# Kernel optimization log

Hardware: AMD Instinct MI355X
Metric: run time of the kernel (lower is better)

The kernel has to match this reference:

```python
import jax, jax.numpy as jnp
import numpy as np

B, S, D, H = 2, 2048, 1024, 16
DEPTH = D // H


def setup_inputs() -> dict:
    key = jax.random.key(0)
    ks = jax.random.split(key, 10)
    scale = 1.0 / np.sqrt(D)
    x = jax.random.normal(ks[0], (B, S, D), dtype=jnp.float32)
    # Astromer-style float mask: values in [0,1], shape (B, S, 1)
    mask = jax.random.uniform(ks[1], (B, S, 1), dtype=jnp.float32)
    Wq = jax.random.normal(ks[2], (D, D), dtype=jnp.float32) * scale
    bq = jnp.zeros((D,), dtype=jnp.float32)
    Wk = jax.random.normal(ks[3], (D, D), dtype=jnp.float32) * scale
    bk = jnp.zeros((D,), dtype=jnp.float32)
    Wv = jax.random.normal(ks[4], (D, D), dtype=jnp.float32) * scale
    bv = jnp.zeros((D,), dtype=jnp.float32)
    Wo = jax.random.normal(ks[5], (D, D), dtype=jnp.float32) * scale
    bo = jnp.zeros((D,), dtype=jnp.float32)
    return {"x": x, "mask": mask, "Wq": Wq, "bq": bq, "Wk": Wk, "bk": bk,
            "Wv": Wv, "bv": bv, "Wo": Wo, "bo": bo}


def _split_heads(t):
    # (B, S, D) -> (B, H, S, depth)
    b, s, _ = t.shape
    return t.reshape(b, s, H, DEPTH).transpose(0, 2, 1, 3)


def reference(x, mask, Wq, bq, Wk, bk, Wv, bv, Wo, bo):
    b, s, d = x.shape
    q = _split_heads(x @ Wq + bq)  # (B,H,S,depth)
    k = _split_heads(x @ Wk + bk)
    v = _split_heads(x @ Wv + bv)
    logits = jnp.einsum('bhqd,bhkd->bhqk', q, k) / jnp.sqrt(
        jnp.asarray(DEPTH, dtype=x.dtype))
    # symmetric mask: tile (B,S,1) -> (B,S,S), add transpose, clamp at 1
    m = jnp.broadcast_to(mask, (b, s, s))  # tile along last dim
    m = m + m.transpose(0, 2, 1)
    m = jnp.minimum(1.0, m)
    logits = logits + m[:, None, :, :]  # broadcast over heads
    attn = jax.nn.softmax(logits, axis=-1)
    z = jnp.einsum('bhqk,bhkd->bhqd', attn, v)
    z = z.transpose(0, 2, 1, 3).reshape(b, s, d)
    out = z @ Wo + bo
    return out, attn
```

## Files before the change

### kernel.cpp

```cpp
#include <hip/hip_runtime.h>

#define B_ 2
#define S_ 2048
#define D_ 1024
#define H_ 16
#define DEPTH_ 64

#define SWZ(g, d) ((((g) ^ ((d) & 15)) << 2))

__global__ __launch_bounds__(256, 2) void gemm128(
    const float* __restrict__ A, const float* __restrict__ Bw,
    const float* __restrict__ bias, float* __restrict__ C)
{
    __shared__ float As[16][132];
    __shared__ float Bs[16][132];
    int t = threadIdx.x;
    int row0 = blockIdx.y * 128, col0 = blockIdx.x * 128;

    int ar = t >> 2, ak = (t & 3) << 2;
    int bk = t >> 5, bc = (t & 31) << 2;
    int tm = (t >> 4) << 3, tn = (t & 15) << 3;

    float acc[8][8] = {};

    for (int k0 = 0; k0 < 1024; k0 += 16) {
        float4 a0 = *(const float4*)(A + (long)(row0 + ar) * 1024 + k0 + ak);
        float4 a1 = *(const float4*)(A + (long)(row0 + ar + 64) * 1024 + k0 + ak);
        float4 b0 = *(const float4*)(Bw + (long)(k0 + bk) * 1024 + col0 + bc);
        float4 b1 = *(const float4*)(Bw + (long)(k0 + bk + 8) * 1024 + col0 + bc);
        As[ak + 0][ar] = a0.x; As[ak + 1][ar] = a0.y;
        As[ak + 2][ar] = a0.z; As[ak + 3][ar] = a0.w;
        As[ak + 0][ar + 64] = a1.x; As[ak + 1][ar + 64] = a1.y;
        As[ak + 2][ar + 64] = a1.z; As[ak + 3][ar + 64] = a1.w;
        *(float4*)&Bs[bk][bc] = b0;
        *(float4*)&Bs[bk + 8][bc] = b1;
        __syncthreads();
#pragma unroll
        for (int kk = 0; kk < 16; ++kk) {
            float4 x0 = *(const float4*)&As[kk][tm];
            float4 x1 = *(const float4*)&As[kk][tm + 4];
            float4 y0 = *(const float4*)&Bs[kk][tn];
            float4 y1 = *(const float4*)&Bs[kk][tn + 4];
            float xa[8] = {x0.x, x0.y, x0.z, x0.w, x1.x, x1.y, x1.z, x1.w};
            float yb[8] = {y0.x, y0.y, y0.z, y0.w, y1.x, y1.y, y1.z, y1.w};
#pragma unroll
            for (int i = 0; i < 8; ++i)
#pragma unroll
                for (int j = 0; j < 8; ++j) acc[i][j] += xa[i] * yb[j];
        }
        __syncthreads();
    }

    float4 bv0 = *(const float4*)(bias + col0 + tn);
    float4 bv1 = *(const float4*)(bias + col0 + tn + 4);
#pragma unroll
    for (int i = 0; i < 8; ++i) {
        float4 o0, o1;
        o0.x = acc[i][0] + bv0.x; o0.y = acc[i][1] + bv0.y;
        o0.z = acc[i][2] + bv0.z; o0.w = acc[i][3] + bv0.w;
        o1.x = acc[i][4] + bv1.x; o1.y = acc[i][5] + bv1.y;
        o1.z = acc[i][6] + bv1.z; o1.w = acc[i][7] + bv1.w;
        float* cp = C + (long)(row0 + tm + i) * 1024 + col0;
        *(float4*)(cp + tn) = o0;
        *(float4*)(cp + tn + 4) = o1;
    }
}

__global__ __launch_bounds__(256, 2) void scores(
    const float* __restrict__ q, const float* __restrict__ k,
    const float* __restrict__ mask, float* __restrict__ attn)
{
    __shared__ float Qs[64 * 64];
    __shared__ float Ks[64 * 64];
    int t = threadIdx.x;
    int bh = blockIdx.z, b = bh >> 4, h = bh & 15;
    int q0 = blockIdx.y * 64, k0 = blockIdx.x * 64;

    int rr = t >> 4, c4 = (t & 15) << 2;
    const float* qb = q + (long)(b * S_ + q0) * D_ + h * DEPTH_;
    const float* kb = k + (long)(b * S_ + k0) * D_ + h * DEPTH_;
#pragma unroll
    for (int i = 0; i < 4; ++i) {
        int r = rr + 16 * i;
        float4 qv = *(const float4*)(qb + (long)r * D_ + c4);
        float4 kv = *(const float4*)(kb + (long)r * D_ + c4);
        int g = r >> 2, e = r & 3;
        Qs[(c4 + 0) * 64 + SWZ(g, c4 + 0) + e] = qv.x;
        Qs[(c4 + 1) * 64 + SWZ(g, c4 + 1) + e] = qv.y;
        Qs[(c4 + 2) * 64 + SWZ(g, c4 + 2) + e] = qv.z;
        Qs[(c4 + 3) * 64 + SWZ(g, c4 + 3) + e] = qv.w;
        Ks[(c4 + 0) * 64 + SWZ(g, c4 + 0) + e] = kv.x;
        Ks[(c4 + 1) * 64 + SWZ(g, c4 + 1) + e] = kv.y;
        Ks[(c4 + 2) * 64 + SWZ(g, c4 + 2) + e] = kv.z;
        Ks[(c4 + 3) * 64 + SWZ(g, c4 + 3) + e] = kv.w;
    }
    __syncthreads();

    int tm = (t >> 4) << 2, tn = (t & 15) << 2;
    int gm = tm >> 2, gn = tn >> 2;
    float acc[4][4] = {};
#pragma unroll
    for (int kk = 0; kk < 64; ++kk) {
        float4 qa = *(const float4*)&Qs[kk * 64 + SWZ(gm, kk)];
        float4 kv = *(const float4*)&Ks[kk * 64 + SWZ(gn, kk)];
        float xa[4] = {qa.x, qa.y, qa.z, qa.w};
        float yb[4] = {kv.x, kv.y, kv.z, kv.w};
#pragma unroll
        for (int i = 0; i < 4; ++i)
#pragma unroll
            for (int j = 0; j < 4; ++j) acc[i][j] += xa[i] * yb[j];
    }

    float mq[4];
#pragma unroll
    for (int i = 0; i < 4; ++i) mq[i] = mask[b * S_ + q0 + tm + i];
    float4 mk4 = *(const float4*)(mask + b * S_ + k0 + tn);
    float mk[4] = {mk4.x, mk4.y, mk4.z, mk4.w};
    float* op = attn + (long)bh * S_ * S_;
#pragma unroll
    for (int i = 0; i < 4; ++i) {
        float4 o;
        o.x = acc[i][0] * 0.125f + fminf(1.0f, mq[i] + mk[0]);
        o.y = acc[i][1] * 0.125f + fminf(1.0f, mq[i] + mk[1]);
        o.z = acc[i][2] * 0.125f + fminf(1.0f, mq[i] + mk[2]);
        o.w = acc[i][3] * 0.125f + fminf(1.0f, mq[i] + mk[3]);
        *(float4*)(op + (long)(q0 + tm + i) * S_ + k0 + tn) = o;
    }
}

__global__ __launch_bounds__(256, 2) void attn_av(
    float* __restrict__ attn, const float* __restrict__ v, float* __restrict__ z)
{
    __shared__ float Ps[64 * 64];
    __shared__ float Vs[64 * 64];
    __shared__ float m_s[64], linv_s[64];

    int t = threadIdx.x;
    int bh = blockIdx.y, b = bh >> 4, h = bh & 15;
    int q0 = blockIdx.x * 64;
    float* arow = attn + (long)bh * S_ * S_;

    int wv = t >> 6, lane = t & 63;
    for (int rr = 0; rr < 16; ++rr) {
        int r = wv * 16 + rr;
        const float* rowp = arow + (long)(q0 + r) * S_;
        float4 x[8];
#pragma unroll
        for (int j = 0; j < 8; ++j)
            x[j] = *(const float4*)(rowp + 4 * lane + 256 * j);
        float m = -1e30f;
#pragma unroll
        for (int j = 0; j < 8; ++j) {
            m = fmaxf(m, fmaxf(fmaxf(x[j].x, x[j].y), fmaxf(x[j].z, x[j].w)));
        }
#pragma unroll
        for (int off = 32; off; off >>= 1) m = fmaxf(m, __shfl_xor(m, off, 64));
        float s = 0.f;
#pragma unroll
        for (int j = 0; j < 8; ++j) {
            s += __expf(x[j].x - m) + __expf(x[j].y - m) +
                 __expf(x[j].z - m) + __expf(x[j].w - m);
        }
#pragma unroll
        for (int off = 32; off; off >>= 1) s += __shfl_xor(s, off, 64);
        if (lane == 0) { m_s[r] = m; linv_s[r] = 1.0f / s; }
    }
    __syncthreads();

    int rr16 = t >> 4, c4 = (t & 15) << 2;
    int tm = (t >> 4) << 2, tn = (t & 15) << 2;
    int gm = tm >> 2;
    float acc[4][4] = {};

    for (int kt = 0; kt < 32; ++kt) {
        int k0 = kt * 64;
#pragma unroll
        for (int i = 0; i < 4; ++i) {
            int r = rr16 + 16 * i;
            float* lp = arow + (long)(q0 + r) * S_ + k0 + c4;
            float4 lg = *(float4*)lp;
            float mm = m_s[r], li = linv_s[r];
            float4 p;
            p.x = __expf(lg.x - mm) * li;
            p.y = __expf(lg.y - mm) * li;
            p.z = __expf(lg.z - mm) * li;
            p.w = __expf(lg.w - mm) * li;
            *(float4*)lp = p;
            int g = r >> 2, e = r & 3;
            Ps[(c4 + 0) * 64 + SWZ(g, c4 + 0) + e] = p.x;
            Ps[(c4 + 1) * 64 + SWZ(g, c4 + 1) + e] = p.y;
            Ps[(c4 + 2) * 64 + SWZ(g, c4 + 2) + e] = p.z;
            Ps[(c4 + 3) * 64 + SWZ(g, c4 + 3) + e] = p.w;
            float4 vv = *(const float4*)(v + (long)(b * S_ + k0 + r) * D_ + h * DEPTH_ + c4);
            *(float4*)&Vs[r * 64 + c4] = vv;
        }
        __syncthreads();
#pragma unroll
        for (int kk = 0; kk < 64; ++kk) {
            float4 pa = *(const float4*)&Ps[kk * 64 + SWZ(gm, kk)];
            float4 vb = *(const float4*)&Vs[kk * 64 + tn];
            float xa[4] = {pa.x, pa.y, pa.z, pa.w};
            float yb[4] = {vb.x, vb.y, vb.z, vb.w};
#pragma unroll
            for (int i = 0; i < 4; ++i)
#pragma unroll
                for (int j = 0; j < 4; ++j) acc[i][j] += xa[i] * yb[j];
        }
        __syncthreads();
    }

#pragma unroll
    for (int i = 0; i < 4; ++i) {
        float4 o;
        o.x = acc[i][0]; o.y = acc[i][1]; o.z = acc[i][2]; o.w = acc[i][3];
        *(float4*)(z + (long)(b * S_ + q0 + tm + i) * D_ + h * DEPTH_ + tn) = o;
    }
}

extern "C" void kernel_launch(void* const* d_in, const int* in_sizes, int n_in,
                              void* d_out, int out_size, void* d_ws, size_t ws_size,
                              hipStream_t stream)
{
    const float* x    = (const float*)d_in[0];
    const float* mask = (const float*)d_in[1];
    const float* Wq   = (const float*)d_in[2];
    const float* bq   = (const float*)d_in[3];
    const float* Wk   = (const float*)d_in[4];
    const float* bk   = (const float*)d_in[5];
    const float* Wv   = (const float*)d_in[6];
    const float* bv   = (const float*)d_in[7];
    const float* Wo   = (const float*)d_in[8];
    const float* bo   = (const float*)d_in[9];

    float* out  = (float*)d_out;
    float* attn = out + (size_t)B_ * S_ * D_;

    size_t n = (size_t)B_ * S_ * D_;
    float* q = (float*)d_ws;
    float* k = q + n;
    float* v = k + n;
    float* z = v + n;

    dim3 blk(256);
    gemm128<<<dim3(8, 32), blk, 0, stream>>>(x, Wq, bq, q);
    gemm128<<<dim3(8, 32), blk, 0, stream>>>(x, Wk, bk, k);
    gemm128<<<dim3(8, 32), blk, 0, stream>>>(x, Wv, bv, v);

    scores<<<dim3(32, 32, 32), blk, 0, stream>>>(q, k, mask, attn);
    attn_av<<<dim3(32, 32), blk, 0, stream>>>(attn, v, z);

    gemm128<<<dim3(8, 32), blk, 0, stream>>>(z, Wo, bo, out);
}
```

Before: 1.840 ms.

## Fuse scores, softmax and AV into two-pass attention kernel; batch QKV GEMMs

Combines the separate scores and attn_av kernels into one kernel. The first pass recomputes QK^T per key tile to build an online max and sum, and the second pass recomputes the logits, writes normalized probabilities with nontemporal stores, and accumulates P·V from shared memory. This avoids writing raw logits to the 512MB attn buffer and reading them back twice, at the cost of computing QK^T twice. It also merges the three QKV projections into one launch via blockIdx.z and adds block-index swizzling and K double-buffering.

```diff
diff --git a/kernel.cpp b/kernel.cpp
--- a/kernel.cpp
+++ b/kernel.cpp
@@ -8,7 +8,9 @@
 
 #define SWZ(g, d) ((((g) ^ ((d) & 15)) << 2))
 
-__global__ __launch_bounds__(256, 2) void gemm128(
+typedef float f4v __attribute__((ext_vector_type(4)));
+
+__device__ __forceinline__ void gemm128_body(
     const float* __restrict__ A, const float* __restrict__ Bw,
     const float* __restrict__ bias, float* __restrict__ C)
 {
@@ -66,145 +68,208 @@
     }
 }
 
-__global__ __launch_bounds__(256, 2) void scores(
+__global__ __launch_bounds__(256, 2) void gemm128(
+    const float* __restrict__ A, const float* __restrict__ Bw,
+    const float* __restrict__ bias, float* __restrict__ C)
+{
+    gemm128_body(A, Bw, bias, C);
+}
+
+__global__ __launch_bounds__(256, 2) void gemm128_qkv(
+    const float* __restrict__ x,
+    const float* __restrict__ Wq, const float* __restrict__ bq,
+    const float* __restrict__ Wk, const float* __restrict__ bk,
+    const float* __restrict__ Wv, const float* __restrict__ bv,
+    float* __restrict__ q, float* __restrict__ k, float* __restrict__ v)
+{
+    const float* Bw; const float* bias; float* C;
+    if (blockIdx.z == 0)      { Bw = Wq; bias = bq; C = q; }
+    else if (blockIdx.z == 1) { Bw = Wk; bias = bk; C = k; }
+    else                      { Bw = Wv; bias = bv; C = v; }
+    gemm128_body(x, Bw, bias, C);
+}
+
+__global__ __launch_bounds__(256, 2) void attn_fused(
     const float* __restrict__ q, const float* __restrict__ k,
-    const float* __restrict__ mask, float* __restrict__ attn)
+    const float* __restrict__ v, const float* __restrict__ mask,
+    float* __restrict__ attn, float* __restrict__ z)
 {
     __shared__ float Qs[64 * 64];
-    __shared__ float Ks[64 * 64];
+    __shared__ float Ka[64 * 64];
+    __shared__ float Kb[64 * 64];
+    __shared__ float Vs[64 * 64];
+
     int t = threadIdx.x;
-    int bh = blockIdx.z, b = bh >> 4, h = bh & 15;
-    int q0 = blockIdx.y * 64, k0 = blockIdx.x * 64;
+    int bid = blockIdx.y * 32 + blockIdx.x;
+    bid = (bid & 7) * 128 + (bid >> 3);
+    int q0 = (bid & 31) * 64;
+    int bh = bid >> 5, b = bh >> 4, h = bh & 15;
 
     int rr = t >> 4, c4 = (t & 15) << 2;
+    int tm = rr << 2, tn = c4;
+    int gm = rr, gn = t & 15;
+
     const float* qb = q + (long)(b * S_ + q0) * D_ + h * DEPTH_;
-    const float* kb = k + (long)(b * S_ + k0) * D_ + h * DEPTH_;
+    const float* kb0 = k + ((long)b * S_) * D_ + h * DEPTH_;
+    const float* vb0 = v + ((long)b * S_) * D_ + h * DEPTH_;
+
 #pragma unroll
     for (int i = 0; i < 4; ++i) {
         int r = rr + 16 * i;
         float4 qv = *(const float4*)(qb + (long)r * D_ + c4);
-        float4 kv = *(const float4*)(kb + (long)r * D_ + c4);
         int g = r >> 2, e = r & 3;
         Qs[(c4 + 0) * 64 + SWZ(g, c4 + 0) + e] = qv.x;
         Qs[(c4 + 1) * 64 + SWZ(g, c4 + 1) + e] = qv.y;
         Qs[(c4 + 2) * 64 + SWZ(g, c4 + 2) + e] = qv.z;
         Qs[(c4 + 3) * 64 + SWZ(g, c4 + 3) + e] = qv.w;
-        Ks[(c4 + 0) * 64 + SWZ(g, c4 + 0) + e] = kv.x;
-        Ks[(c4 + 1) * 64 + SWZ(g, c4 + 1) + e] = kv.y;
-        Ks[(c4 + 2) * 64 + SWZ(g, c4 + 2) + e] = kv.z;
-        Ks[(c4 + 3) * 64 + SWZ(g, c4 + 3) + e] = kv.w;
-    }
-    __syncthreads();
-
-    int tm = (t >> 4) << 2, tn = (t & 15) << 2;
-    int gm = tm >> 2, gn = tn >> 2;
-    float acc[4][4] = {};
-#pragma unroll
-    for (int kk = 0; kk < 64; ++kk) {
-        float4 qa = *(const float4*)&Qs[kk * 64 + SWZ(gm, kk)];
-        float4 kv = *(const float4*)&Ks[kk * 64 + SWZ(gn, kk)];
-        float xa[4] = {qa.x, qa.y, qa.z, qa.w};
-        float yb[4] = {kv.x, kv.y, kv.z, kv.w};
-#pragma unroll
-        for (int i = 0; i < 4; ++i)
-#pragma unroll
-            for (int j = 0; j < 4; ++j) acc[i][j] += xa[i] * yb[j];
     }
 
     float mq[4];
 #pragma unroll
     for (int i = 0; i < 4; ++i) mq[i] = mask[b * S_ + q0 + tm + i];
-    float4 mk4 = *(const float4*)(mask + b * S_ + k0 + tn);
-    float mk[4] = {mk4.x, mk4.y, mk4.z, mk4.w};
-    float* op = attn + (long)bh * S_ * S_;
+
+    float m_run[4] = {-1e30f, -1e30f, -1e30f, -1e30f};
+    float l_run[4] = {0.f, 0.f, 0.f, 0.f};
+
+    float4 kreg[4], vreg[4];
+#pragma unroll
+    for (int i = 0; i < 4; ++i)
+        kreg[i] = *(const float4*)(kb0 + (long)(rr + 16 * i) * D_ + c4);
 #pragma unroll
     for (int i = 0; i < 4; ++i) {
-        float4 o;
-        o.x = acc[i][0] * 0.125f + fminf(1.0f, mq[i] + mk[0]);
-        o.y = acc[i][1] * 0.125f + fminf(1.0f, mq[i] + mk[1]);
-        o.z = acc[i][2] * 0.125f + fminf(1.0f, mq[i] + mk[2]);
-        o.w = acc[i][3] * 0.125f + fminf(1.0f, mq[i] + mk[3]);
-        *(float4*)(op + (long)(q0 + tm + i) * S_ + k0 + tn) = o;
-    }
-}
-
-__global__ __launch_bounds__(256, 2) void attn_av(
-    float* __restrict__ attn, const float* __restrict__ v, float* __restrict__ z)
-{
-    __shared__ float Ps[64 * 64];
-    __shared__ float Vs[64 * 64];
-    __shared__ float m_s[64], linv_s[64];
-
-    int t = threadIdx.x;
-    int bh = blockIdx.y, b = bh >> 4, h = bh & 15;
-    int q0 = blockIdx.x * 64;
+        int r = rr + 16 * i, g = r >> 2, e = r & 3;
+        Ka[(c4 + 0) * 64 + SWZ(g, c4 + 0) + e] = kreg[i].x;
+        Ka[(c4 + 1) * 64 + SWZ(g, c4 + 1) + e] = kreg[i].y;
+        Ka[(c4 + 2) * 64 + SWZ(g, c4 + 2) + e] = kreg[i].z;
+        Ka[(c4 + 3) * 64 + SWZ(g, c4 + 3) + e] = kreg[i].w;
+    }
+
+    for (int kt = 0; kt < 32; ++kt) {
+        __syncthreads();
+        if (kt < 31) {
+            const float* kp = kb0 + (long)(kt + 1) * 64 * D_;
+#pragma unroll
+            for (int i = 0; i < 4; ++i)
+                kreg[i] = *(const float4*)(kp + (long)(rr + 16 * i) * D_ + c4);
+        }
+        const float* KT = (kt & 1) ? Kb : Ka;
+        float acc[4][4] = {};
+#pragma unroll
+        for (int kk = 0; kk < 64; ++kk) {
+            float4 qa = *(const float4*)&Qs[kk * 64 + SWZ(gm, kk)];
+            float4 kv = *(const float4*)&KT[kk * 64 + SWZ(gn, kk)];
+            float xa[4] = {qa.x, qa.y, qa.z, qa.w};
+            float yb[4] = {kv.x, kv.y, kv.z, kv.w};
+#pragma unroll
+            for (int i = 0; i < 4; ++i)
+#pragma unroll
+                for (int j = 0; j < 4; ++j) acc[i][j] += xa[i] * yb[j];
+        }
+        float4 mk4 = *(const float4*)(mask + b * S_ + kt * 64 + tn);
+        float mk[4] = {mk4.x, mk4.y, mk4.z, mk4.w};
+#pragma unroll
+        for (int i = 0; i < 4; ++i) {
+            float lg[4];
+#pragma unroll
+            for (int j = 0; j < 4; ++j)
+                lg[j] = acc[i][j] * 0.125f + fminf(1.0f, mq[i] + mk[j]);
+            float tmax = fmaxf(fmaxf(lg[0], lg[1]), fmaxf(lg[2], lg[3]));
+#pragma unroll
+            for (int off = 8; off; off >>= 1)
+                tmax = fmaxf(tmax, __shfl_xor(tmax, off, 64));
+            float s = __expf(lg[0] - tmax) + __expf(lg[1] - tmax) +
+                      __expf(lg[2] - tmax) + __expf(lg[3] - tmax);
+#pragma unroll
+            for (int off = 8; off; off >>= 1) s += __shfl_xor(s, off, 64);
+            float mnew = fmaxf(m_run[i], tmax);
+            l_run[i] = l_run[i] * __expf(m_run[i] - mnew) + s * __expf(tmax - mnew);
+            m_run[i] = mnew;
+        }
+        if (kt < 31) {
+            float* KT2 = (kt & 1) ? Ka : Kb;
+#pragma unroll
+            for (int i = 0; i < 4; ++i) {
+                int r = rr + 16 * i, g = r >> 2, e = r & 3;
+                KT2[(c4 + 0) * 64 + SWZ(g, c4 + 0) + e] = kreg[i].x;
+                KT2[(c4 + 1) * 64 + SWZ(g, c4 + 1) + e] = kreg[i].y;
+                KT2[(c4 + 2) * 64 + SWZ(g, c4 + 2) + e] = kreg[i].z;
+                KT2[(c4 + 3) * 64 + SWZ(g, c4 + 3) + e] = kreg[i].w;
+            }
+        }
+    }
+
+    float linv[4];
+#pragma unroll
+    for (int i = 0; i < 4; ++i) linv[i] = 1.0f / l_run[i];
+
     float* arow = attn + (long)bh * S_ * S_;
-
-    int wv = t >> 6, lane = t & 63;
-    for (int rr = 0; rr < 16; ++rr) {
-        int r = wv * 16 + rr;
-        const float* rowp = arow + (long)(q0 + r) * S_;
-        float4 x[8];
-#pragma unroll
-        for (int j = 0; j < 8; ++j)
-            x[j] = *(const float4*)(rowp + 4 * lane + 256 * j);
-        float m = -1e30f;
-#pragma unroll
-        for (int j = 0; j < 8; ++j) {
-            m = fmaxf(m, fmaxf(fmaxf(x[j].x, x[j].y), fmaxf(x[j].z, x[j].w)));
-        }
-#pragma unroll
-        for (int off = 32; off; off >>= 1) m = fmaxf(m, __shfl_xor(m, off, 64));
-        float s = 0.f;
-#pragma unroll
-        for (int j = 0; j < 8; ++j) {
-            s += __expf(x[j].x - m) + __expf(x[j].y - m) +
-                 __expf(x[j].z - m) + __expf(x[j].w - m);
-        }
-#pragma unroll
-        for (int off = 32; off; off >>= 1) s += __shfl_xor(s, off, 64);
-        if (lane == 0) { m_s[r] = m; linv_s[r] = 1.0f / s; }
-    }
-    __syncthreads();
-
-    int rr16 = t >> 4, c4 = (t & 15) << 2;
-    int tm = (t >> 4) << 2, tn = (t & 15) << 2;
-    int gm = tm >> 2;
-    float acc[4][4] = {};
+    float zacc[4][4] = {};
+
+#pragma unroll
+    for (int i = 0; i < 4; ++i) {
+        kreg[i] = *(const float4*)(kb0 + (long)(rr + 16 * i) * D_ + c4);
+        vreg[i] = *(const float4*)(vb0 + (long)(rr + 16 * i) * D_ + c4);
+    }
 
     for (int kt = 0; kt < 32; ++kt) {
-        int k0 = kt * 64;
 #pragma unroll
         for (int i = 0; i < 4; ++i) {
-            int r = rr16 + 16 * i;
-            float* lp = arow + (long)(q0 + r) * S_ + k0 + c4;
-            float4 lg = *(float4*)lp;
-            float mm = m_s[r], li = linv_s[r];
-            float4 p;
-            p.x = __expf(lg.x - mm) * li;
-            p.y = __expf(lg.y - mm) * li;
-            p.z = __expf(lg.z - mm) * li;
-            p.w = __expf(lg.w - mm) * li;
-            *(float4*)lp = p;
-            int g = r >> 2, e = r & 3;
-            Ps[(c4 + 0) * 64 + SWZ(g, c4 + 0) + e] = p.x;
-            Ps[(c4 + 1) * 64 + SWZ(g, c4 + 1) + e] = p.y;
-            Ps[(c4 + 2) * 64 + SWZ(g, c4 + 2) + e] = p.z;
-            Ps[(c4 + 3) * 64 + SWZ(g, c4 + 3) + e] = p.w;
-            float4 vv = *(const float4*)(v + (long)(b * S_ + k0 + r) * D_ + h * DEPTH_ + c4);
-            *(float4*)&Vs[r * 64 + c4] = vv;
-        }
-        __syncthreads();
+            int r = rr + 16 * i, g = r >> 2, e = r & 3;
+            Ka[(c4 + 0) * 64 + SWZ(g, c4 + 0) + e] = kreg[i].x;
+            Ka[(c4 + 1) * 64 + SWZ(g, c4 + 1) + e] = kreg[i].y;
+            Ka[(c4 + 2) * 64 + SWZ(g, c4 + 2) + e] = kreg[i].z;
+            Ka[(c4 + 3) * 64 + SWZ(g, c4 + 3) + e] = kreg[i].w;
+            *(float4*)&Vs[r * 64 + c4] = vreg[i];
+        }
+        __syncthreads();
+        if (kt < 31) {
+            const float* kp = kb0 + (long)(kt + 1) * 64 * D_;
+            const float* vp = vb0 + (long)(kt + 1) * 64 * D_;
+#pragma unroll
+            for (int i = 0; i < 4; ++i) {
+                kreg[i] = *(const float4*)(kp + (long)(rr + 16 * i) * D_ + c4);
+                vreg[i] = *(const float4*)(vp + (long)(rr + 16 * i) * D_ + c4);
+            }
+        }
+        float acc[4][4] = {};
 #pragma unroll
         for (int kk = 0; kk < 64; ++kk) {
-            float4 pa = *(const float4*)&Ps[kk * 64 + SWZ(gm, kk)];
+            float4 qa = *(const float4*)&Qs[kk * 64 + SWZ(gm, kk)];
+            float4 kv = *(const float4*)&Ka[kk * 64 + SWZ(gn, kk)];
+            float xa[4] = {qa.x, qa.y, qa.z, qa.w};
+            float yb[4] = {kv.x, kv.y, kv.z, kv.w};
+#pragma unroll
+            for (int i = 0; i < 4; ++i)
+#pragma unroll
+                for (int j = 0; j < 4; ++j) acc[i][j] += xa[i] * yb[j];
+        }
+        float4 mk4 = *(const float4*)(mask + b * S_ + kt * 64 + tn);
+#pragma unroll
+        for (int i = 0; i < 4; ++i) {
+            float4 o;
+            o.x = __expf(acc[i][0] * 0.125f + fminf(1.0f, mq[i] + mk4.x) - m_run[i]) * linv[i];
+            o.y = __expf(acc[i][1] * 0.125f + fminf(1.0f, mq[i] + mk4.y) - m_run[i]) * linv[i];
+            o.z = __expf(acc[i][2] * 0.125f + fminf(1.0f, mq[i] + mk4.z) - m_run[i]) * linv[i];
+            o.w = __expf(acc[i][3] * 0.125f + fminf(1.0f, mq[i] + mk4.w) - m_run[i]) * linv[i];
+            f4v ov = {o.x, o.y, o.z, o.w};
+            __builtin_nontemporal_store(
+                ov, (f4v*)(arow + (long)(q0 + tm + i) * S_ + kt * 64 + tn));
+            Kb[(tn + 0) * 64 + SWZ(gm, tn + 0) + i] = o.x;
+            Kb[(tn + 1) * 64 + SWZ(gm, tn + 1) + i] = o.y;
+            Kb[(tn + 2) * 64 + SWZ(gm, tn + 2) + i] = o.z;
+            Kb[(tn + 3) * 64 + SWZ(gm, tn + 3) + i] = o.w;
+        }
+        __syncthreads();
+#pragma unroll
+        for (int kk = 0; kk < 64; ++kk) {
+            float4 pa = *(const float4*)&Kb[kk * 64 + SWZ(gm, kk)];
             float4 vb = *(const float4*)&Vs[kk * 64 + tn];
             float xa[4] = {pa.x, pa.y, pa.z, pa.w};
             float yb[4] = {vb.x, vb.y, vb.z, vb.w};
 #pragma unroll
             for (int i = 0; i < 4; ++i)
 #pragma unroll
-                for (int j = 0; j < 4; ++j) acc[i][j] += xa[i] * yb[j];
+                for (int j = 0; j < 4; ++j) zacc[i][j] += xa[i] * yb[j];
         }
         __syncthreads();
     }
@@ -212,7 +277,7 @@
 #pragma unroll
     for (int i = 0; i < 4; ++i) {
         float4 o;
-        o.x = acc[i][0]; o.y = acc[i][1]; o.z = acc[i][2]; o.w = acc[i][3];
+        o.x = zacc[i][0]; o.y = zacc[i][1]; o.z = zacc[i][2]; o.w = zacc[i][3];
         *(float4*)(z + (long)(b * S_ + q0 + tm + i) * D_ + h * DEPTH_ + tn) = o;
     }
 }
@@ -242,12 +307,8 @@
     float* z = v + n;
 
     dim3 blk(256);
-    gemm128<<<dim3(8, 32), blk, 0, stream>>>(x, Wq, bq, q);
-    gemm128<<<dim3(8, 32), blk, 0, stream>>>(x, Wk, bk, k);
-    gemm128<<<dim3(8, 32), blk, 0, stream>>>(x, Wv, bv, v);
-
-    scores<<<dim3(32, 32, 32), blk, 0, stream>>>(q, k, mask, attn);
-    attn_av<<<dim3(32, 32), blk, 0, stream>>>(attn, v, z);
-
+    gemm128_qkv<<<dim3(8, 32, 3), blk, 0, stream>>>(x, Wq, bq, Wk, bk, Wv, bv,
+                                                    q, k, v);
+    attn_fused<<<dim3(32, 32), blk, 0, stream>>>(q, k, v, mask, attn, z);
     gemm128<<<dim3(8, 32), blk, 0, stream>>>(z, Wo, bo, out);
 }
```

After: 1.861 ms. Within noise of the previous version (+1.1%).
